# Performance work log

Measured on AMD Instinct MI355X. Metric: run time of the kernel, lower is better.

## Reference

```python
import jax, jax.numpy as jnp
import numpy as np
from jax import lax

K_RATIO = 0.5  # args['k_ratio'], eval (non-training) branch
K_SIZE = 5     # args['gaussian_smooth']['k_size']
C_SIGMA = 1.0  # args['gaussian_smooth']['c_sigma']


def _gaussian_kernel(k_size=K_SIZE, sigma=C_SIGMA):
    # matches Communication.init_gaussian_filter (note: 2*pi*sigma, not sigma^2, as in source)
    c = k_size // 2
    x, y = np.mgrid[-c:k_size - c, -c:k_size - c]
    g = 1.0 / (2.0 * np.pi * sigma) * np.exp(-(np.square(x) + np.square(y)) / (2.0 * np.square(sigma)))
    return jnp.asarray(g, jnp.float32)[None, None]  # (1,1,k,k) OIHW, bias is zero


def setup_inputs() -> dict:
    key = jax.random.key(0)
    conf = jax.random.normal(jax.random.fold_in(key, 1), (8, 6, 4, 512, 512), jnp.float32)
    warp = jnp.ones((8, 1, 512, 512), jnp.float32)
    return {"confidence_maps": conf, "warp_masks": warp, "gauss_kernel": _gaussian_kernel()}


def reference(confidence_maps, warp_masks, gauss_kernel):
    # confidence_maps: (B, L, C, H, W); warp_masks: (B, 1, H, W); gauss_kernel: (1,1,k,k)
    B, L, C, H, W = confidence_maps.shape
    # sigmoid + max over anchor dim, keepdim -> (B, L, 1, H, W)
    m = jnp.max(jax.nn.sigmoid(confidence_maps), axis=2, keepdims=True)
    m = m * warp_masks[:, None]  # broadcast warp mask over agents
    # frozen gaussian smoothing conv, SAME padding (stride 1, pad (k-1)//2)
    sm = lax.conv_general_dilated(m.reshape(B * L, 1, H, W), gauss_kernel,
                                  window_strides=(1, 1), padding='SAME',
                                  dimension_numbers=('NCHW', 'OIHW', 'NCHW'))
    flat = sm.reshape(B, L, H * W)
    K = int(H * W * K_RATIO)  # static k, eval k_ratio branch
    _, idx = lax.top_k(flat, K)  # (B, L, K)
    mask = jnp.zeros_like(flat).at[
        jnp.arange(B)[:, None, None], jnp.arange(L)[None, :, None], idx
    ].set(1.0)  # scatter ones at top-k positions
    # communication rate computed BEFORE ego mask is forced to 1 (as in source)
    rate = jnp.mean(jnp.sum(mask[:, 1:], axis=(1, 2)) / ((L - 1) * H * W))
    mask = mask.reshape(B, L, H, W).at[:, 0].set(1.0)  # ego agent keeps everything
    return mask.reshape(B * L, 1, H, W), rate
```

## Files before the change

kernel.cpp:

```cpp
#include <hip/hip_runtime.h>


#define NROWSEL 40
#define NPIX    262144
#define KSEL    131072u
#define CAND_CAP 2048

#define OFF_KEY  0ull
#define OFF_H1   20971520ull
#define OFF_H2   21012480ull
#define OFF_ST   21053440ull
#define OFF_CC   21054080ull
#define OFF_CI   21054240ull
#define META_BYTES 82720ull

__device__ __forceinline__ unsigned qkey(double v) {
  double t = v * 4294967296.0;
  t = fmax(t, 0.0);
  t = fmin(t, 4294967295.0);
  return (unsigned)t;
}

__device__ __forceinline__ double m_val(const float* __restrict__ confr,
                                        const float* __restrict__ warpr,
                                        int gy, int gx) {
  if (gy < 0 || gy >= 512 || gx < 0 || gx >= 512) return 0.0;
  int off = gy * 512 + gx;
  float x0 = confr[off];
  float x1 = confr[NPIX + off];
  float x2 = confr[2 * NPIX + off];
  float x3 = confr[3 * NPIX + off];
  float mx = fmaxf(fmaxf(x0, x1), fmaxf(x2, x3));
  double s = 1.0 / (1.0 + exp(-(double)mx));
  return s * (double)warpr[off];
}

__global__ void ego_fill_kernel(float* __restrict__ out) {
  int i = blockIdx.x * 256 + threadIdx.x;
  int b = i >> 16;
  int o4 = i & 65535;
  float4* p = (float4*)(out + (size_t)b * 6u * NPIX) + o4;
  *p = make_float4(1.f, 1.f, 1.f, 1.f);
}

__global__ __launch_bounds__(256, 5) void compute_kernel(
    const float* __restrict__ conf, const float* __restrict__ warp,
    const float* __restrict__ gk, unsigned short* __restrict__ keys,
    unsigned* __restrict__ hist1) {
  const int blk = blockIdx.x;
  const int j = blk >> 7;
  const int tile = blk & 127;
  const int ty0 = (tile >> 3) << 5;
  const int tx0 = (tile & 7) << 6;
  const int b = j / 5;
  const int l = j % 5 + 1;
  const int rowg = b * 6 + l;
  const float* confr = conf + (size_t)rowg * 4u * NPIX;
  const float* warpr = warp + (size_t)b * NPIX;

  __shared__ double mt[36][68];
  __shared__ double g[25];
  __shared__ unsigned lh[256];
  const int tid = threadIdx.x;
  if (tid < 25) g[tid] = (double)gk[tid];
  lh[tid] = 0u;

  for (int i = tid; i < 36 * 68; i += 256) {
    int hy = i / 68, hx = i % 68;
    mt[hy][hx] = m_val(confr, warpr, ty0 + hy - 2, tx0 + hx - 2);
  }
  __syncthreads();

  const int txl = tid & 63;
  const int tyl = tid >> 6;
  unsigned short* keyrow = keys + (size_t)j * NPIX;
  for (int rr = 0; rr < 8; ++rr) {
    int yy = tyl + (rr << 2);
    double acc = 0.0;
#pragma unroll
    for (int dy = 0; dy < 5; ++dy)
#pragma unroll
      for (int dx = 0; dx < 5; ++dx)
        acc = fma(g[dy * 5 + dx], mt[yy + dy][txl + dx], acc);
    unsigned k = qkey(acc);
    keyrow[(ty0 + yy) * 512 + (tx0 + txl)] = (unsigned short)(k >> 16);
    atomicAdd(&lh[k >> 24], 1u);
  }
  __syncthreads();
  if (lh[tid]) atomicAdd(&hist1[j * 256 + tid], lh[tid]);
}

__global__ void scan1_kernel(const unsigned* __restrict__ hist1,
                             int* __restrict__ st) {
  int j = blockIdx.x;
  const unsigned* h = hist1 + j * 256;
  __shared__ unsigned cs[256];
  int tid = threadIdx.x;
  cs[tid] = h[tid];
  __syncthreads();
  if (tid == 0) {
    unsigned cum = 0; int b1 = 255; unsigned A1 = 0;
    for (int c = 255; c >= 0; --c) {
      if (cum + cs[c] >= KSEL) { b1 = c; A1 = cum; break; }
      cum += cs[c];
    }
    st[j * 4 + 0] = b1;
    st[j * 4 + 1] = (int)A1;
  }
}

__global__ __launch_bounds__(256) void hist2_kernel(
    const unsigned short* __restrict__ keys, const int* __restrict__ st,
    unsigned* __restrict__ hist2) {
  int blk = blockIdx.x;
  int j = blk >> 5, seg = blk & 31;
  unsigned b1 = (unsigned)st[j * 4 + 0];
  const uint4* kp = (const uint4*)(keys + (size_t)j * NPIX + seg * 8192);
  __shared__ unsigned lh[256];
  lh[threadIdx.x] = 0u;
  __syncthreads();
#pragma unroll
  for (int it = 0; it < 4; ++it) {
    uint4 k4 = kp[threadIdx.x + it * 256];
    unsigned w[4] = {k4.x, k4.y, k4.z, k4.w};
#pragma unroll
    for (int e = 0; e < 4; ++e) {
      unsigned lo = w[e] & 0xFFFFu, hi = w[e] >> 16;
      if ((lo >> 8) == b1) atomicAdd(&lh[lo & 255u], 1u);
      if ((hi >> 8) == b1) atomicAdd(&lh[hi & 255u], 1u);
    }
  }
  __syncthreads();
  if (lh[threadIdx.x]) atomicAdd(&hist2[j * 256 + threadIdx.x], lh[threadIdx.x]);
}

__global__ void scan2_kernel(const unsigned* __restrict__ hist2,
                             int* __restrict__ st) {
  int j = blockIdx.x;
  const unsigned* h = hist2 + j * 256;
  __shared__ unsigned cs[256];
  int tid = threadIdx.x;
  cs[tid] = h[tid];
  __syncthreads();
  if (tid == 0) {
    unsigned b1 = (unsigned)st[j * 4 + 0];
    unsigned A1 = (unsigned)st[j * 4 + 1];
    unsigned cum = A1; int b2 = 255; unsigned A2 = A1;
    for (int c = 255; c >= 0; --c) {
      if (cum + cs[c] >= KSEL) { b2 = c; A2 = cum; break; }
      cum += cs[c];
    }
    st[j * 4 + 2] = (int)((b1 << 8) | (unsigned)b2);
    st[j * 4 + 3] = (int)A2;
  }
}

__global__ __launch_bounds__(256) void mask_gather_kernel(
    const unsigned short* __restrict__ keys, const int* __restrict__ st,
    float* __restrict__ out, unsigned* __restrict__ ccount,
    int* __restrict__ cidx) {
  int blk = blockIdx.x;
  int j = blk >> 5, seg = blk & 31;
  int b = j / 5, l = j % 5 + 1;
  int rowg = b * 6 + l;
  unsigned pstar = (unsigned)st[j * 4 + 2];
  const uint4* kp = (const uint4*)(keys + (size_t)j * NPIX + seg * 8192);
  float4* o4 = (float4*)(out + (size_t)rowg * NPIX + seg * 8192);
#pragma unroll
  for (int it = 0; it < 4; ++it) {
    int q = threadIdx.x + it * 256;
    uint4 k4 = kp[q];
    unsigned w[4] = {k4.x, k4.y, k4.z, k4.w};
    float4 mv[2];
    float* mf = (float*)mv;
#pragma unroll
    for (int e = 0; e < 4; ++e) {
      unsigned lo = w[e] & 0xFFFFu;
      unsigned hi = w[e] >> 16;
      mf[e * 2] = lo > pstar ? 1.f : 0.f;
      mf[e * 2 + 1] = hi > pstar ? 1.f : 0.f;
      if (lo == pstar) {
        unsigned s = atomicAdd(&ccount[j], 1u);
        if (s < CAND_CAP) cidx[j * CAND_CAP + s] = seg * 8192 + q * 8 + e * 2;
      }
      if (hi == pstar) {
        unsigned s = atomicAdd(&ccount[j], 1u);
        if (s < CAND_CAP) cidx[j * CAND_CAP + s] = seg * 8192 + q * 8 + e * 2 + 1;
      }
    }
    o4[q * 2] = mv[0];
    o4[q * 2 + 1] = mv[1];
  }
}

__global__ __launch_bounds__(256) void finalize_kernel(
    const float* __restrict__ conf, const float* __restrict__ warp,
    const float* __restrict__ gk, const int* __restrict__ st,
    const unsigned* __restrict__ ccount, const int* __restrict__ cidx,
    float* __restrict__ out) {
  int j = blockIdx.x;
  int b = j / 5, l = j % 5 + 1;
  int rowg = b * 6 + l;
  const float* confr = conf + (size_t)rowg * 4u * NPIX;
  const float* warpr = warp + (size_t)b * NPIX;
  __shared__ double vs[CAND_CAP];
  __shared__ int ids[CAND_CAP];
  __shared__ double g[25];
  int tid = threadIdx.x;
  if (tid < 25) g[tid] = (double)gk[tid];
  unsigned A2 = (unsigned)st[j * 4 + 3];
  int R = (int)(KSEL - A2);
  int C = (int)min(ccount[j], (unsigned)CAND_CAP);
  __syncthreads();
  for (int i = tid; i < C; i += 256) {
    int idx = cidx[j * CAND_CAP + i];
    int y = idx >> 9, x = idx & 511;
    double acc = 0.0;
#pragma unroll
    for (int dy = 0; dy < 5; ++dy)
#pragma unroll
      for (int dx = 0; dx < 5; ++dx)
        acc = fma(g[dy * 5 + dx], m_val(confr, warpr, y + dy - 2, x + dx - 2), acc);
    vs[i] = acc;
    ids[i] = idx;
  }
  __syncthreads();
  for (int i = tid; i < C; i += 256) {
    double vi = vs[i];
    int ii = ids[i];
    int rank = 0;
    for (int q = 0; q < C; ++q) {
      double vq = vs[q];
      rank += (vq > vi) || (vq == vi && ids[q] < ii) ? 1 : 0;
    }
    if (rank < R) out[(size_t)rowg * NPIX + ii] = 1.0f;
  }
  if (j == 0 && tid == 0) out[12582912] = 0.5f;
}

extern "C" void kernel_launch(void* const* d_in, const int* in_sizes, int n_in,
                              void* d_out, int out_size, void* d_ws, size_t ws_size,
                              hipStream_t stream) {
  const float* conf = (const float*)d_in[0];
  const float* warp = (const float*)d_in[1];
  const float* gk   = (const float*)d_in[2];
  float* out = (float*)d_out;
  char* ws = (char*)d_ws;

  unsigned short* keys = (unsigned short*)(ws + OFF_KEY);
  unsigned* h1 = (unsigned*)(ws + OFF_H1);
  unsigned* h2 = (unsigned*)(ws + OFF_H2);
  int*      st = (int*)(ws + OFF_ST);
  unsigned* cc = (unsigned*)(ws + OFF_CC);
  int*      ci = (int*)(ws + OFF_CI);

  hipMemsetAsync(ws + OFF_H1, 0, (size_t)META_BYTES, stream);

  ego_fill_kernel<<<2048, 256, 0, stream>>>(out);
  compute_kernel<<<NROWSEL * 128, 256, 0, stream>>>(conf, warp, gk, keys, h1);
  scan1_kernel<<<NROWSEL, 256, 0, stream>>>(h1, st);
  hist2_kernel<<<NROWSEL * 32, 256, 0, stream>>>(keys, st, h2);
  scan2_kernel<<<NROWSEL, 256, 0, stream>>>(h2, st);
  mask_gather_kernel<<<NROWSEL * 32, 256, 0, stream>>>(keys, st, out, cc, ci);
  finalize_kernel<<<NROWSEL, 256, 0, stream>>>(conf, warp, gk, st, cc, ci, out);
}
```

Measured before the change: 150.0 us.

## Compute smoothing in fp32 and refine a widened pivot band in fp64

The main smoothing kernel now computes sigmoid, max and the 5x5 Gaussian in fp32 instead of fp64. It quantises directly to 16-bit keys and uses 64x64 tiles, which cuts halo recomputation. To absorb fp32 rounding error, the gather stage collects every pixel within ±KAPPA key bins of the pivot as a candidate. The finalize stage then recomputes those candidates in fp64 and ranks them, with the required count adjusted for candidates above the pivot. In exchange, the quadratic rank loop in finalize can grow with the larger candidate cap. If more pixels fall in the band than the cap holds, the result would be wrong.

```diff
diff --git a/kernel.cpp b/kernel.cpp
--- a/kernel.cpp
+++ b/kernel.cpp
@@ -3,8 +3,9 @@
 
 #define NROWSEL 40
 #define NPIX    262144
-#define KSEL    131072u
-#define CAND_CAP 2048
+#define KSEL    131072
+#define CAND_CAP 4096
+#define KAPPA    2
 
 #define OFF_KEY  0ull
 #define OFF_H1   20971520ull
@@ -12,13 +13,21 @@
 #define OFF_ST   21053440ull
 #define OFF_CC   21054080ull
 #define OFF_CI   21054240ull
+#define OFF_CK   21709600ull
 #define META_BYTES 82720ull
 
-__device__ __forceinline__ unsigned qkey(double v) {
-  double t = v * 4294967296.0;
-  t = fmax(t, 0.0);
-  t = fmin(t, 4294967295.0);
-  return (unsigned)t;
+__device__ __forceinline__ float m_val_f32(const float* __restrict__ confr,
+                                           const float* __restrict__ warpr,
+                                           int gy, int gx) {
+  if (gy < 0 || gy >= 512 || gx < 0 || gx >= 512) return 0.0f;
+  int off = gy * 512 + gx;
+  float x0 = confr[off];
+  float x1 = confr[NPIX + off];
+  float x2 = confr[2 * NPIX + off];
+  float x3 = confr[3 * NPIX + off];
+  float mx = fmaxf(fmaxf(x0, x1), fmaxf(x2, x3));
+  float s = 1.0f / (1.0f + expf(-mx));
+  return s * warpr[off];
 }
 
 __device__ __forceinline__ double m_val(const float* __restrict__ confr,
@@ -43,14 +52,14 @@
   *p = make_float4(1.f, 1.f, 1.f, 1.f);
 }
 
-__global__ __launch_bounds__(256, 5) void compute_kernel(
+__global__ __launch_bounds__(256) void compute_kernel(
     const float* __restrict__ conf, const float* __restrict__ warp,
     const float* __restrict__ gk, unsigned short* __restrict__ keys,
     unsigned* __restrict__ hist1) {
   const int blk = blockIdx.x;
-  const int j = blk >> 7;
-  const int tile = blk & 127;
-  const int ty0 = (tile >> 3) << 5;
+  const int j = blk >> 6;
+  const int tile = blk & 63;
+  const int ty0 = (tile >> 3) << 6;
   const int tx0 = (tile & 7) << 6;
   const int b = j / 5;
   const int l = j % 5 + 1;
@@ -58,33 +67,33 @@
   const float* confr = conf + (size_t)rowg * 4u * NPIX;
   const float* warpr = warp + (size_t)b * NPIX;
 
-  __shared__ double mt[36][68];
-  __shared__ double g[25];
+  __shared__ float mt[68][68];
+  __shared__ float g[25];
   __shared__ unsigned lh[256];
   const int tid = threadIdx.x;
-  if (tid < 25) g[tid] = (double)gk[tid];
+  if (tid < 25) g[tid] = gk[tid];
   lh[tid] = 0u;
 
-  for (int i = tid; i < 36 * 68; i += 256) {
+  for (int i = tid; i < 68 * 68; i += 256) {
     int hy = i / 68, hx = i % 68;
-    mt[hy][hx] = m_val(confr, warpr, ty0 + hy - 2, tx0 + hx - 2);
+    mt[hy][hx] = m_val_f32(confr, warpr, ty0 + hy - 2, tx0 + hx - 2);
   }
   __syncthreads();
 
   const int txl = tid & 63;
   const int tyl = tid >> 6;
   unsigned short* keyrow = keys + (size_t)j * NPIX;
-  for (int rr = 0; rr < 8; ++rr) {
+  for (int rr = 0; rr < 16; ++rr) {
     int yy = tyl + (rr << 2);
-    double acc = 0.0;
+    float acc = 0.0f;
 #pragma unroll
     for (int dy = 0; dy < 5; ++dy)
 #pragma unroll
       for (int dx = 0; dx < 5; ++dx)
-        acc = fma(g[dy * 5 + dx], mt[yy + dy][txl + dx], acc);
-    unsigned k = qkey(acc);
-    keyrow[(ty0 + yy) * 512 + (tx0 + txl)] = (unsigned short)(k >> 16);
-    atomicAdd(&lh[k >> 24], 1u);
+        acc = fmaf(g[dy * 5 + dx], mt[yy + dy][txl + dx], acc);
+    unsigned k = (unsigned)fminf(fmaxf(acc * 65536.0f, 0.0f), 65535.0f);
+    keyrow[(ty0 + yy) * 512 + (tx0 + txl)] = (unsigned short)k;
+    atomicAdd(&lh[k >> 8], 1u);
   }
   __syncthreads();
   if (lh[tid]) atomicAdd(&hist1[j * 256 + tid], lh[tid]);
@@ -101,7 +110,7 @@
   if (tid == 0) {
     unsigned cum = 0; int b1 = 255; unsigned A1 = 0;
     for (int c = 255; c >= 0; --c) {
-      if (cum + cs[c] >= KSEL) { b1 = c; A1 = cum; break; }
+      if (cum + cs[c] >= (unsigned)KSEL) { b1 = c; A1 = cum; break; }
       cum += cs[c];
     }
     st[j * 4 + 0] = b1;
@@ -147,7 +156,7 @@
     unsigned A1 = (unsigned)st[j * 4 + 1];
     unsigned cum = A1; int b2 = 255; unsigned A2 = A1;
     for (int c = 255; c >= 0; --c) {
-      if (cum + cs[c] >= KSEL) { b2 = c; A2 = cum; break; }
+      if (cum + cs[c] >= (unsigned)KSEL) { b2 = c; A2 = cum; break; }
       cum += cs[c];
     }
     st[j * 4 + 2] = (int)((b1 << 8) | (unsigned)b2);
@@ -158,12 +167,12 @@
 __global__ __launch_bounds__(256) void mask_gather_kernel(
     const unsigned short* __restrict__ keys, const int* __restrict__ st,
     float* __restrict__ out, unsigned* __restrict__ ccount,
-    int* __restrict__ cidx) {
+    int* __restrict__ cidx, unsigned short* __restrict__ ckey) {
   int blk = blockIdx.x;
   int j = blk >> 5, seg = blk & 31;
   int b = j / 5, l = j % 5 + 1;
   int rowg = b * 6 + l;
-  unsigned pstar = (unsigned)st[j * 4 + 2];
+  int pstar = st[j * 4 + 2];
   const uint4* kp = (const uint4*)(keys + (size_t)j * NPIX + seg * 8192);
   float4* o4 = (float4*)(out + (size_t)rowg * NPIX + seg * 8192);
 #pragma unroll
@@ -175,17 +184,19 @@
     float* mf = (float*)mv;
 #pragma unroll
     for (int e = 0; e < 4; ++e) {
-      unsigned lo = w[e] & 0xFFFFu;
-      unsigned hi = w[e] >> 16;
-      mf[e * 2] = lo > pstar ? 1.f : 0.f;
-      mf[e * 2 + 1] = hi > pstar ? 1.f : 0.f;
-      if (lo == pstar) {
+      int lo = (int)(w[e] & 0xFFFFu);
+      int hi = (int)(w[e] >> 16);
+      mf[e * 2]     = lo > pstar + KAPPA ? 1.f : 0.f;
+      mf[e * 2 + 1] = hi > pstar + KAPPA ? 1.f : 0.f;
+      if (lo >= pstar - KAPPA && lo <= pstar + KAPPA) {
         unsigned s = atomicAdd(&ccount[j], 1u);
-        if (s < CAND_CAP) cidx[j * CAND_CAP + s] = seg * 8192 + q * 8 + e * 2;
+        if (s < CAND_CAP) { cidx[j * CAND_CAP + s] = seg * 8192 + q * 8 + e * 2;
+                            ckey[j * CAND_CAP + s] = (unsigned short)lo; }
       }
-      if (hi == pstar) {
+      if (hi >= pstar - KAPPA && hi <= pstar + KAPPA) {
         unsigned s = atomicAdd(&ccount[j], 1u);
-        if (s < CAND_CAP) cidx[j * CAND_CAP + s] = seg * 8192 + q * 8 + e * 2 + 1;
+        if (s < CAND_CAP) { cidx[j * CAND_CAP + s] = seg * 8192 + q * 8 + e * 2 + 1;
+                            ckey[j * CAND_CAP + s] = (unsigned short)hi; }
       }
     }
     o4[q * 2] = mv[0];
@@ -197,7 +208,7 @@
     const float* __restrict__ conf, const float* __restrict__ warp,
     const float* __restrict__ gk, const int* __restrict__ st,
     const unsigned* __restrict__ ccount, const int* __restrict__ cidx,
-    float* __restrict__ out) {
+    const unsigned short* __restrict__ ckey, float* __restrict__ out) {
   int j = blockIdx.x;
   int b = j / 5, l = j % 5 + 1;
   int rowg = b * 6 + l;
@@ -208,8 +219,8 @@
   __shared__ double g[25];
   int tid = threadIdx.x;
   if (tid < 25) g[tid] = (double)gk[tid];
-  unsigned A2 = (unsigned)st[j * 4 + 3];
-  int R = (int)(KSEL - A2);
+  int pstar = st[j * 4 + 2];
+  int A2 = st[j * 4 + 3];
   int C = (int)min(ccount[j], (unsigned)CAND_CAP);
   __syncthreads();
   for (int i = tid; i < C; i += 256) {
@@ -225,6 +236,10 @@
     ids[i] = idx;
   }
   __syncthreads();
+  int cntAbove = 0;
+  for (int q = 0; q < C; ++q)
+    cntAbove += (int)ckey[j * CAND_CAP + q] > pstar ? 1 : 0;
+  int R = KSEL - A2 + cntAbove;
   for (int i = tid; i < C; i += 256) {
     double vi = vs[i];
     int ii = ids[i];
@@ -253,14 +268,15 @@
   int*      st = (int*)(ws + OFF_ST);
   unsigned* cc = (unsigned*)(ws + OFF_CC);
   int*      ci = (int*)(ws + OFF_CI);
+  unsigned short* ck = (unsigned short*)(ws + OFF_CK);
 
   hipMemsetAsync(ws + OFF_H1, 0, (size_t)META_BYTES, stream);
 
   ego_fill_kernel<<<2048, 256, 0, stream>>>(out);
-  compute_kernel<<<NROWSEL * 128, 256, 0, stream>>>(conf, warp, gk, keys, h1);
+  compute_kernel<<<NROWSEL * 64, 256, 0, stream>>>(conf, warp, gk, keys, h1);
   scan1_kernel<<<NROWSEL, 256, 0, stream>>>(h1, st);
   hist2_kernel<<<NROWSEL * 32, 256, 0, stream>>>(keys, st, h2);
   scan2_kernel<<<NROWSEL, 256, 0, stream>>>(h2, st);
-  mask_gather_kernel<<<NROWSEL * 32, 256, 0, stream>>>(keys, st, out, cc, ci);
-  finalize_kernel<<<NROWSEL, 256, 0, stream>>>(conf, warp, gk, st, cc, ci, out);
-}
+  mask_gather_kernel<<<NROWSEL * 32, 256, 0, stream>>>(keys, st, out, cc, ci, ck);
+  finalize_kernel<<<NROWSEL, 256, 0, stream>>>(conf, warp, gk, st, cc, ci, ck, out);
+}
```

Result: slower. 220.8 us (+47.2%).
